# Performance work log

Hardware: AMD Instinct MI355X
Metric: run time of the kernel (lower is better)

Reference implementation:

```python
import jax, jax.numpy as jnp
import numpy as np

S, B, I, H, NH, HD, ML = 512, 32, 768, 256, 8, 32, 512
LN_EPS = 1e-5


def setup_inputs() -> dict:
    key = jax.random.key(0)
    ks = jax.random.split(key, 12)
    r = lambda k, shp, s=0.05: jax.random.normal(k, shp, dtype=jnp.float32) * s
    return {
        'x': r(ks[0], (S, B, I), 1.0),
        'Wi': r(ks[1], (5 * H, I)), 'bi': jnp.zeros((5 * H,), jnp.float32),
        'Wh': r(ks[2], (5 * H, H)), 'bh': jnp.zeros((5 * H,), jnp.float32),
        'Wt': r(ks[3], (H, 3 * H)), 'bt': jnp.zeros((H,), jnp.float32),
        'Wq': r(ks[4], (3, H, H)), 'bq': jnp.zeros((3, H), jnp.float32),
        'Wk': r(ks[5], (3, H, H)), 'bk': jnp.zeros((3, H), jnp.float32),
        'Wv': r(ks[6], (3, H, H)), 'bv': jnp.zeros((3, H), jnp.float32),
        'Wo': r(ks[7], (3, H, H)), 'bo': jnp.zeros((3, H), jnp.float32),
        'relpos': r(ks[8], (3, NH, ML, HD), 1.0),
        'ln_g': jnp.ones((H,), jnp.float32), 'ln_b': jnp.zeros((H,), jnp.float32),
    }


def cumsoftmax(z):
    return jnp.cumsum(jax.nn.softmax(z, axis=-1), axis=-1)


def _forward(x, Wi, bi, Wh, bh, Wt, bt, Wq, bq, Wk, bk, Wv, bv, Wo, bo, relpos, ln_g, ln_b):
    # --- sequential PFN (ON-LSTM style) recurrence over time ---
    def step(carry, xt):
        h, c_in = carry
        gates = xt @ Wi.T + bi + h @ Wh.T + bh            # [B, 5H]
        c, eg_cin, rg_cin, eg_c, rg_c = jnp.split(gates, 5, axis=-1)
        eg_cin = 1.0 - cumsoftmax(eg_cin)
        rg_cin = cumsoftmax(rg_cin)
        eg_c = 1.0 - cumsoftmax(eg_c)
        rg_c = cumsoftmax(rg_c)
        c = jnp.tanh(c)
        ov_c = rg_c * eg_c
        up_c = rg_c - ov_c
        dn_c = eg_c - ov_c
        ov_i = rg_cin * eg_cin
        up_i = rg_cin - ov_i
        dn_i = eg_cin - ov_i
        share = ov_i * c_in + ov_c * c
        c_re = up_i * c_in + up_c * c + share
        c_ner = dn_i * c_in + dn_c * c + share
        h_re = jnp.tanh(c_re)
        h_ner = jnp.tanh(c_ner)
        h_share = jnp.tanh(share)
        c_out = jnp.concatenate([c_re, c_ner, share], axis=-1) @ Wt.T + bt
        h_out = jnp.tanh(c_out)
        return (h_out, c_out), (h_ner, h_re, h_share)

    init = (jnp.zeros((B, H), x.dtype), jnp.zeros((B, H), x.dtype))
    _, (h_ner, h_re, h_share) = jax.lax.scan(step, init, x)   # each [S, B, H]

    # --- relative multi-head attention (no 1/sqrt(d) scaling, as in source) ---
    def attn(hb, i):
        b, s, d = hb.shape
        q = (hb @ Wq[i].T + bq[i]).reshape(b, s, NH, HD)
        k = (hb @ Wk[i].T + bk[i]).reshape(b, s, NH, HD)
        v = (hb @ Wv[i].T + bv[i]).reshape(b, s, NH, HD)
        scores = jnp.einsum('bqnd,bknd->bnqk', q, k) \
               + jnp.einsum('bqnd,nkd->bnqk', q, relpos[i][:, :s])
        w = jax.nn.softmax(scores, axis=-1)
        o = jnp.einsum('bnqk,bknd->bqnd', w, v).reshape(b, s, d)
        return o @ Wo[i].T + bo[i]

    def layer_norm(z):
        m = z.mean(-1, keepdims=True)
        v = z.var(-1, keepdims=True)
        return (z - m) / jnp.sqrt(v + LN_EPS) * ln_g + ln_b

    def apply_attention(h_sbd, i):
        hb = jnp.transpose(h_sbd, (1, 0, 2))      # [B, S, H]
        y = layer_norm(hb + attn(hb, i))          # residual + LN (dropout=0, eval)
        return jnp.transpose(y, (1, 0, 2))        # back to [S, B, H]

    out_ner = apply_attention(h_ner, 0)
    out_re = apply_attention(h_re, 1)
    out_share = apply_attention(h_re, 2)  # faithful to source: h_share attn consumes h_re
    return out_ner, out_re, out_share


def reference(x, Wi, bi, Wh, bh, Wt, bt, Wq, bq, Wk, bk, Wv, bv, Wo, bo, relpos, ln_g, ln_b):
    return _forward(x, Wi, bi, Wh, bh, Wt, bt, Wq, bq, Wk, bk, Wv, bv, Wo, bo, relpos, ln_g, ln_b)
```

## Files before the change

kernel.cpp:

```cpp
#include <hip/hip_runtime.h>
#include <hip/hip_bf16.h>

#define SDIM 512
#define BDIM 32

typedef _Float16 v2h __attribute__((ext_vector_type(2)));
typedef short bf16x8 __attribute__((ext_vector_type(8)));
typedef float f32x4 __attribute__((ext_vector_type(4)));

__device__ __forceinline__ float b2f(ushort u) {
    union { uint32_t i; float f; } v; v.i = ((uint32_t)u) << 16; return v.f;
}
__device__ __forceinline__ ushort f2b(float f) {
    union { float f; uint32_t i; } v; v.f = f;
    uint32_t u = v.i;
    return (ushort)((u + 0x7fffu + ((u >> 16) & 1u)) >> 16);
}
__device__ __forceinline__ ushort f2h(float f) {
    union { _Float16 h; ushort u; } v; v.h = (_Float16)f; return v.u;
}
__device__ __forceinline__ float dot2(uint32_t w, uint32_t h, float acc) {
#if __has_builtin(__builtin_amdgcn_fdot2)
    union { uint32_t u; v2h v; } a, b;
    a.u = w; b.u = h;
    return __builtin_amdgcn_fdot2(a.v, b.v, acc, false);
#else
    union { uint32_t u; v2h v; } a, b;
    a.u = w; b.u = h;
    return acc + (float)a.v.x * (float)b.v.x + (float)a.v.y * (float)b.v.y;
#endif
}
__device__ __forceinline__ float ftanh(float x) {
    const float t = __expf(2.f * x);
    return 1.f - 2.f * __builtin_amdgcn_rcpf(t + 1.f);
}

#define DCHUNK8C(WQ, HQ, ACC)                                                  \
    {                                                                          \
        uint4 wA = *(const uint4*)(WQ);                                        \
        uint4 wB = *(const uint4*)((WQ) + 4);                                  \
        uint4 hA = *(const uint4*)(HQ);                                        \
        uint4 hB = *(const uint4*)((HQ) + 4);                                  \
        ACC = dot2(wA.x, hA.x, ACC);                                           \
        ACC = dot2(wA.y, hA.y, ACC);                                           \
        ACC = dot2(wA.z, hA.z, ACC);                                           \
        ACC = dot2(wA.w, hA.w, ACC);                                           \
        ACC = dot2(wB.x, hB.x, ACC);                                           \
        ACC = dot2(wB.y, hB.y, ACC);                                           \
        ACC = dot2(wB.z, hB.z, ACC);                                           \
        ACC = dot2(wB.w, hB.w, ACC);                                           \
    }

__global__ __launch_bounds__(256) void pack8d_kernel(
    const float* __restrict__ src, int ld, uint32_t* __restrict__ out, int P, int J)
{
    const int idx = blockIdx.x * 256 + threadIdx.x;
    if (idx >= P * J) return;
    const int j = idx / P, p = idx - j * P;
    const ushort lo = f2h(src[(size_t)j * ld + 2 * p]);
    const ushort hi = f2h(src[(size_t)j * ld + 2 * p + 1]);
    out[(((size_t)(p >> 3) * J + j) << 3) + (p & 7)] = ((uint32_t)hi << 16) | lo;
}

__global__ __launch_bounds__(256) void cvt_bf16x2_kernel(
    const float* __restrict__ a, ushort* __restrict__ oa, int na,
    const float* __restrict__ b, ushort* __restrict__ ob, int nb)
{
    const int stride = gridDim.x * 256;
    for (int i = blockIdx.x * 256 + threadIdx.x; i < na + nb; i += stride) {
        if (i < na) oa[i] = f2b(a[i]);
        else ob[i - na] = f2b(b[i - na]);
    }
}
__global__ __launch_bounds__(256) void cvt_bf16x4_kernel(
    const float* __restrict__ a, const float* __restrict__ b,
    const float* __restrict__ c, const float* __restrict__ d,
    ushort* __restrict__ oa, ushort* __restrict__ ob,
    ushort* __restrict__ oc, ushort* __restrict__ od, int n)
{
    const int i = blockIdx.x * 256 + threadIdx.x;
    if (i >= 4 * n) return;
    const int which = i / n, j = i - which * n;
    const float* s = which == 0 ? a : which == 1 ? b : which == 2 ? c : d;
    ushort* o = which == 0 ? oa : which == 1 ? ob : which == 2 ? oc : od;
    o[j] = f2b(s[j]);
}

__global__ __launch_bounds__(256) void addvec_kernel(
    const float* __restrict__ a, const float* __restrict__ b,
    float* __restrict__ o, int n)
{
    const int i = blockIdx.x * 256 + threadIdx.x;
    if (i < n) o[i] = a[i] + b[i];
}

__global__ __launch_bounds__(256) void mfma_gemm128_kernel(
    const ushort* __restrict__ A16, const ushort* __restrict__ B16,
    const float* __restrict__ bias, float* __restrict__ C, int N, int K)
{
    __shared__ ushort As[128][72];
    __shared__ ushort Bs[64][72];
    const int tid = threadIdx.x;
    const int tile_m = blockIdx.x * 128, tile_n = blockIdx.y * 64;
    const int ra = tid >> 1, ca = (tid & 1) * 32;
    const int rb = tid >> 2, cb = (tid & 3) * 16;
    const int w = tid >> 6, lane = tid & 63;
    const int mi = lane & 15, quad = lane >> 4;
    f32x4 acc[2][4] = {};

    for (int k0 = 0; k0 < K; k0 += 64) {
        const uint4* ap = (const uint4*)(A16 + (size_t)(tile_m + ra) * K + k0 + ca);
        *(uint4*)&As[ra][ca]      = ap[0];
        *(uint4*)&As[ra][ca + 8]  = ap[1];
        *(uint4*)&As[ra][ca + 16] = ap[2];
        *(uint4*)&As[ra][ca + 24] = ap[3];
        const uint4* bp = (const uint4*)(B16 + (size_t)(tile_n + rb) * K + k0 + cb);
        *(uint4*)&Bs[rb][cb]     = bp[0];
        *(uint4*)&Bs[rb][cb + 8] = bp[1];
        __syncthreads();
        #pragma unroll
        for (int kk = 0; kk < 64; kk += 32) {
            const bf16x8 af0 = *(const bf16x8*)&As[w * 32 + mi][quad * 8 + kk];
            const bf16x8 af1 = *(const bf16x8*)&As[w * 32 + 16 + mi][quad * 8 + kk];
            #pragma unroll
            for (int j = 0; j < 4; j++) {
                const bf16x8 bf = *(const bf16x8*)&Bs[j * 16 + mi][quad * 8 + kk];
                acc[0][j] = __builtin_amdgcn_mfma_f32_16x16x32_bf16(af0, bf, acc[0][j], 0, 0, 0);
                acc[1][j] = __builtin_amdgcn_mfma_f32_16x16x32_bf16(af1, bf, acc[1][j], 0, 0, 0);
            }
        }
        __syncthreads();
    }
    #pragma unroll
    for (int j = 0; j < 4; j++) {
        const int gn = tile_n + j * 16 + mi;
        const float bv = bias[gn];
        #pragma unroll
        for (int f = 0; f < 2; f++) {
            #pragma unroll
            for (int rr = 0; rr < 4; rr++) {
                const int gm = tile_m + w * 32 + f * 16 + quad * 4 + rr;
                C[(size_t)gm * N + gn] = acc[f][j][rr] + bv;
            }
        }
    }
}

__global__ __launch_bounds__(256) void qkv_gemm128_kernel(
    const ushort* __restrict__ A16,
    const ushort* __restrict__ Wq, const ushort* __restrict__ Wk,
    const ushort* __restrict__ Wv,
    const float* __restrict__ bq, const float* __restrict__ bk,
    const float* __restrict__ bv, const float* __restrict__ rp,
    float* __restrict__ qo, float* __restrict__ ko, float* __restrict__ vo)
{
    __shared__ ushort As[128][72];
    __shared__ ushort Bs[3][64][72];
    const int tid = threadIdx.x;
    const int tile_m = blockIdx.x * 128, tile_n = blockIdx.y * 64;
    const int ra = tid >> 1, ca = (tid & 1) * 32;
    const int am = tile_m + ra;
    const int ar = (am & (SDIM - 1)) * BDIM + (am >> 9);
    const int rb = tid >> 2, cb = (tid & 3) * 16;
    const int bn = tile_n + rb;
    const int w = tid >> 6, lane = tid & 63;
    const int mi = lane & 15, quad = lane >> 4;
    f32x4 acc[3][2][4] = {};

    for (int k0 = 0; k0 < 256; k0 += 64) {
        const uint4* ap = (const uint4*)(A16 + (size_t)ar * 256 + k0 + ca);
        *(uint4*)&As[ra][ca]      = ap[0];
        *(uint4*)&As[ra][ca + 8]  = ap[1];
        *(uint4*)&As[ra][ca + 16] = ap[2];
        *(uint4*)&As[ra][ca + 24] = ap[3];
        const uint4* qp = (const uint4*)(Wq + (size_t)bn * 256 + k0 + cb);
        *(uint4*)&Bs[0][rb][cb]     = qp[0];
        *(uint4*)&Bs[0][rb][cb + 8] = qp[1];
        const uint4* kp = (const uint4*)(Wk + (size_t)bn * 256 + k0 + cb);
        *(uint4*)&Bs[1][rb][cb]     = kp[0];
        *(uint4*)&Bs[1][rb][cb + 8] = kp[1];
        const uint4* vp = (const uint4*)(Wv + (size_t)bn * 256 + k0 + cb);
        *(uint4*)&Bs[2][rb][cb]     = vp[0];
        *(uint4*)&Bs[2][rb][cb + 8] = vp[1];
        __syncthreads();
        #pragma unroll
        for (int kk = 0; kk < 64; kk += 32) {
            const bf16x8 af0 = *(const bf16x8*)&As[w * 32 + mi][quad * 8 + kk];
            const bf16x8 af1 = *(const bf16x8*)&As[w * 32 + 16 + mi][quad * 8 + kk];
            #pragma unroll
            for (int z = 0; z < 3; z++) {
                #pragma unroll
                for (int j = 0; j < 4; j++) {
                    const bf16x8 bf = *(const bf16x8*)&Bs[z][j * 16 + mi][quad * 8 + kk];
                    acc[z][0][j] = __builtin_amdgcn_mfma_f32_16x16x32_bf16(af0, bf, acc[z][0][j], 0, 0, 0);
                    acc[z][1][j] = __builtin_amdgcn_mfma_f32_16x16x32_bf16(af1, bf, acc[z][1][j], 0, 0, 0);
                }
            }
        }
        __syncthreads();
    }
    #pragma unroll
    for (int z = 0; z < 3; z++) {
        const float* bias = (z == 0) ? bq : (z == 1) ? bk : bv;
        float* out = (z == 0) ? qo : (z == 1) ? ko : vo;
        #pragma unroll
        for (int j = 0; j < 4; j++) {
            const int gn = tile_n + j * 16 + mi;
            const float bb = bias[gn];
            #pragma unroll
            for (int f = 0; f < 2; f++) {
                #pragma unroll
                for (int rr = 0; rr < 4; rr++) {
                    const int gm = tile_m + w * 32 + f * 16 + quad * 4 + rr;
                    float v = acc[z][f][j][rr] + bb;
                    if (z == 1) {
                        const int sgm = gm & (SDIM - 1);
                        v += rp[((gn >> 5) << 14) + (sgm << 5) + (gn & 31)];
                    }
                    out[(size_t)gm * 256 + gn] = v;
                }
            }
        }
    }
}

__global__ __launch_bounds__(1024) void scan_kernel(
    const float* __restrict__ gx,
    const uint32_t* __restrict__ Wh8,
    const uint32_t* __restrict__ Wt8,
    const float* __restrict__ bt,
    ushort* __restrict__ h_ner,
    ushort* __restrict__ h_re)
{
    const int b = blockIdx.x;
    const int tid = threadIdx.x;
    __shared__ float cs[256], g[1280], ext[1024];
    __shared__ alignas(16) uint32_t hs_pk[128];
    __shared__ alignas(16) uint32_t cat_pk[384];
    __shared__ float rsum[16];
    if (tid < 256) cs[tid] = 0.f;
    if (tid < 128) hs_pk[tid] = 0u;
    __syncthreads();
    const int lane = tid & 63;
    const int ch = tid >> 8;
    const int wch = (tid >> 6) & 3;
    const int er = tid & 255;
    const int ep = tid >> 8;
    const uint32_t* wmain = Wh8 + (size_t)tid * 8;
    const uint32_t* wext  = Wh8 + ((size_t)(ep * 4) * 1280 + 1024 + er) * 8;
    const uint32_t* wtp   = Wt8 + ((size_t)(ep * 12) * 256 + er) * 8;

    for (int t = 0; t < SDIM; t++) {
        const float* gxr = gx + (size_t)(t * BDIM + b) * 1280;
        {
            float a0 = 0.f, a1 = 0.f;
            #pragma unroll 2
            for (int q8 = 0; q8 < 16; q8 += 2) {
                DCHUNK8C(wmain + (size_t)q8 * (1280 * 8), hs_pk + q8 * 8, a0);
                DCHUNK8C(wmain + (size_t)(q8 + 1) * (1280 * 8), hs_pk + q8 * 8 + 8, a1);
            }
            g[tid] = gxr[tid] + a0 + a1;
        }
        {
            float ae = (ep == 0) ? gxr[1024 + er] : 0.f;
            #pragma unroll
            for (int i = 0; i < 4; i++)
                DCHUNK8C(wext + (size_t)i * (1280 * 8), hs_pk + (ep * 4 + i) * 8, ae);
            ext[ep * 256 + er] = ae;
        }
        __syncthreads();
        if (tid < 256) g[tid] = ftanh(g[tid]);
        float v;
        if (tid >= 768) {
            const int r_ = tid - 768;
            v = ext[r_] + ext[256 + r_] + ext[512 + r_] + ext[768 + r_];
        } else {
            v = g[256 + tid];
        }
        const float e = __expf(v);
        float wsum = e;
        #pragma unroll
        for (int off = 32; off >= 1; off >>= 1) wsum += __shfl_xor(wsum, off, 64);
        if (lane == 0) rsum[ch * 4 + wch] = wsum;
        float cum = e;
        #pragma unroll
        for (int off = 1; off <= 32; off <<= 1) {
            float tsh = __shfl_up(cum, (unsigned)off, 64);
            if (lane >= off) cum += tsh;
        }
        __syncthreads();
        const float tot = rsum[ch * 4] + rsum[ch * 4 + 1] + rsum[ch * 4 + 2] + rsum[ch * 4 + 3];
        float prev = 0.f;
        if (wch > 0) prev += rsum[ch * 4];
        if (wch > 1) prev += rsum[ch * 4 + 1];
        if (wch > 2) prev += rsum[ch * 4 + 2];
        float r = (cum + prev) * __builtin_amdgcn_rcpf(tot);
        if (ch == 0 || ch == 2) r = 1.f - r;
        g[256 + tid] = r;
        __syncthreads();
        if (tid < 256) {
            const float c = g[tid];
            const float egi = g[256 + tid], rgi = g[512 + tid];
            const float egc = g[768 + tid], rgc = g[1024 + tid];
            const float cin = cs[tid];
            const float ovc = rgc * egc, upc = rgc - ovc, dnc = egc - ovc;
            const float ovi = rgi * egi, upi = rgi - ovi, dni = egi - ovi;
            const float share = ovi * cin + ovc * c;
            const float cre = upi * cin + upc * c + share;
            const float cner = dni * cin + dnc * c + share;
            ((_Float16*)cat_pk)[tid]       = (_Float16)cre;
            ((_Float16*)cat_pk)[256 + tid] = (_Float16)cner;
            ((_Float16*)cat_pk)[512 + tid] = (_Float16)share;
            const size_t ob = (size_t)(t * BDIM + b) * 256 + tid;
            h_re[ob] = f2b(ftanh(cre));
            h_ner[ob] = f2b(ftanh(cner));
        }
        __syncthreads();
        {
            float s0 = 0.f, s1 = 0.f;
            #pragma unroll 2
            for (int i = 0; i < 12; i += 2) {
                DCHUNK8C(wtp + (size_t)i * (256 * 8), cat_pk + (ep * 12 + i) * 8, s0);
                DCHUNK8C(wtp + (size_t)(i + 1) * (256 * 8), cat_pk + (ep * 12 + i + 1) * 8, s1);
            }
            g[ep * 256 + er] = s0 + s1;
        }
        __syncthreads();
        if (tid < 256) {
            const float co = g[tid] + g[256 + tid] + g[512 + tid] + g[768 + tid] + bt[tid];
            cs[tid] = co;
            ((_Float16*)hs_pk)[tid] = (_Float16)ftanh(co);
        }
        __syncthreads();
    }
}

__global__ __launch_bounds__(512) void attn_kernel(
    const float* __restrict__ q_ws, const float* __restrict__ kk_ws,
    const float* __restrict__ v_ws, ushort* __restrict__ o16)
{
    __shared__ float sc[8 * 516];
    __shared__ float ps[8 * 256];
    __shared__ float sinv[8];
    const int bn = blockIdx.x;
    const int b = bn >> 3, n = bn & 7;
    const int tid = threadIdx.x;
    const int w = tid >> 6, lane = tid & 63;
    const int ki = w * 64 + lane;
    float kv[32];
    {
        const float4* kp = (const float4*)(kk_ws + (size_t)(b * 512 + ki) * 256 + n * 32);
        #pragma unroll
        for (int d4 = 0; d4 < 8; d4++) {
            float4 x = kp[d4];
            kv[4 * d4] = x.x; kv[4 * d4 + 1] = x.y; kv[4 * d4 + 2] = x.z; kv[4 * d4 + 3] = x.w;
        }
    }
    const int rr = lane >> 3, dq = lane & 7;

    for (int q0 = 0; q0 < 512; q0 += 8) {
        const float* qbase = q_ws + (size_t)(b * 512 + q0) * 256 + n * 32;
        #pragma unroll 1
        for (int r = 0; r < 8; r++) {
            const float4* q4 = (const float4*)(qbase + r * 256);
            float s0 = 0.f, s1 = 0.f;
            #pragma unroll
            for (int d4 = 0; d4 < 8; d4 += 2) {
                const float4 qa = q4[d4];
                const float4 qb = q4[d4 + 1];
                s0 += qa.x * kv[4 * d4] + qa.y * kv[4 * d4 + 1]
                    + qa.z * kv[4 * d4 + 2] + qa.w * kv[4 * d4 + 3];
                s1 += qb.x * kv[4 * d4 + 4] + qb.y * kv[4 * d4 + 5]
                    + qb.z * kv[4 * d4 + 6] + qb.w * kv[4 * d4 + 7];
            }
            sc[r * 516 + ki] = s0 + s1;
        }
        __syncthreads();
        {
            float* row = sc + w * 516;
            float4 a = ((const float4*)row)[lane];
            float4 c4 = ((const float4*)row)[lane + 64];
            float mx = fmaxf(fmaxf(fmaxf(a.x, a.y), fmaxf(a.z, a.w)),
                             fmaxf(fmaxf(c4.x, c4.y), fmaxf(c4.z, c4.w)));
            #pragma unroll
            for (int off = 32; off >= 1; off >>= 1) mx = fmaxf(mx, __shfl_xor(mx, off, 64));
            a.x = __expf(a.x - mx); a.y = __expf(a.y - mx);
            a.z = __expf(a.z - mx); a.w = __expf(a.w - mx);
            c4.x = __expf(c4.x - mx); c4.y = __expf(c4.y - mx);
            c4.z = __expf(c4.z - mx); c4.w = __expf(c4.w - mx);
            float sm = a.x + a.y + a.z + a.w + c4.x + c4.y + c4.z + c4.w;
            #pragma unroll
            for (int off = 32; off >= 1; off >>= 1) sm += __shfl_xor(sm, off, 64);
            ((float4*)row)[lane] = a;
            ((float4*)row)[lane + 64] = c4;
            if (lane == 0) sinv[w] = 1.f / sm;
        }
        __syncthreads();
        {
            float4 acc0 = {0.f, 0.f, 0.f, 0.f};
            float4 acc1 = {0.f, 0.f, 0.f, 0.f};
            const float* erow = sc + rr * 516 + w * 64;
            const float* vbase = v_ws + (size_t)(b * 512 + w * 64) * 256 + n * 32 + dq * 4;
            #pragma unroll 4
            for (int j = 0; j < 64; j += 2) {
                const float e0 = erow[j], e1 = erow[j + 1];
                float4 v0 = *(const float4*)(vbase + (size_t)j * 256);
                float4 v1 = *(const float4*)(vbase + (size_t)(j + 1) * 256);
                acc0.x += e0 * v0.x; acc0.y += e0 * v0.y;
                acc0.z += e0 * v0.z; acc0.w += e0 * v0.w;
                acc1.x += e1 * v1.x; acc1.y += e1 * v1.y;
                acc1.z += e1 * v1.z; acc1.w += e1 * v1.w;
            }
            float4 acc = {acc0.x + acc1.x, acc0.y + acc1.y,
                          acc0.z + acc1.z, acc0.w + acc1.w};
            ((float4*)ps)[tid] = acc;
        }
        __syncthreads();
        if (tid < 256) {
            const int r2 = tid >> 5, d = tid & 31;
            float s = 0.f;
            #pragma unroll
            for (int ww = 0; ww < 8; ww++) s += ps[ww * 256 + r2 * 32 + d];
            o16[(size_t)(b * 512 + q0 + r2) * 256 + n * 32 + d] = f2b(s * sinv[r2]);
        }
        __syncthreads();
    }
}

__global__ __launch_bounds__(256) void ln_kernel(
    const float* __restrict__ proj, const ushort* __restrict__ hsrc,
    const float* __restrict__ lng, const float* __restrict__ lnb,
    float* __restrict__ outp)
{
    const int m = blockIdx.x;
    const int j = threadIdx.x;
    const int b = m >> 9, s = m & 511;
    const size_t oidx = (size_t)(s * 32 + b) * 256 + j;
    const float y = proj[(size_t)m * 256 + j] + b2f(hsrc[oidx]);
    float sum = y, sq = y * y;
    #pragma unroll
    for (int off = 32; off >= 1; off >>= 1) {
        sum += __shfl_xor(sum, off, 64);
        sq += __shfl_xor(sq, off, 64);
    }
    __shared__ float r1[4], r2[4];
    const int wv = j >> 6;
    if ((j & 63) == 0) { r1[wv] = sum; r2[wv] = sq; }
    __syncthreads();
    const float ts = r1[0] + r1[1] + r1[2] + r1[3];
    const float tq = r2[0] + r2[1] + r2[2] + r2[3];
    const float mean = ts * (1.f / 256.f);
    const float var = tq * (1.f / 256.f) - mean * mean;
    const float o = (y - mean) * rsqrtf(var + 1e-5f) * lng[j] + lnb[j];
    outp[oidx] = o;
}

extern "C" void kernel_launch(void* const* d_in, const int* in_sizes, int n_in,
                              void* d_out, int out_size, void* d_ws, size_t ws_size,
                              hipStream_t stream) {
    (void)in_sizes; (void)n_in; (void)out_size; (void)ws_size;
    const float* x   = (const float*)d_in[0];
    const float* Wi  = (const float*)d_in[1];
    const float* bi  = (const float*)d_in[2];
    const float* Wh  = (const float*)d_in[3];
    const float* bh  = (const float*)d_in[4];
    const float* Wt  = (const float*)d_in[5];
    const float* bt  = (const float*)d_in[6];
    const float* Wq  = (const float*)d_in[7];
    const float* bq  = (const float*)d_in[8];
    const float* Wk  = (const float*)d_in[9];
    const float* bk  = (const float*)d_in[10];
    const float* Wv  = (const float*)d_in[11];
    const float* bv  = (const float*)d_in[12];
    const float* Wo  = (const float*)d_in[13];
    const float* bo  = (const float*)d_in[14];
    const float* rp  = (const float*)d_in[15];
    const float* lng = (const float*)d_in[16];
    const float* lnb = (const float*)d_in[17];
    float* outp = (float*)d_out;

    float* ws = (float*)d_ws;
    float* gx    = ws;
    float* q_ws  = ws;
    float* kk_ws = ws + 4194304;
    float* v_ws  = ws + 8388608;
    float* pj_ws = ws + 12582912;
    ushort* o16  = (ushort*)(ws + 16777216);
    ushort* hner16 = (ushort*)(ws + 20971520);
    ushort* hre16  = (ushort*)(ws + 23068672);
    uint32_t* Wh8 = (uint32_t*)(ws + 25165824);
    uint32_t* Wt8 = (uint32_t*)(ws + 25329664);
    ushort* Wq16 = (ushort*)(ws + 25427968);
    ushort* Wk16 = (ushort*)(ws + 25526272);
    ushort* Wv16 = (ushort*)(ws + 25624576);
    ushort* Wo16 = (ushort*)(ws + 25722880);

    ushort* x16  = (ushort*)outp;
    ushort* Wi16 = (ushort*)(outp + 6291456);
    float* bsum  = outp + 7307264;

    pack8d_kernel<<<dim3(640), 256, 0, stream>>>(Wh, 256, Wh8, 128, 1280);
    pack8d_kernel<<<dim3(384), 256, 0, stream>>>(Wt, 768, Wt8, 384, 256);
    addvec_kernel<<<dim3(5), 256, 0, stream>>>(bi, bh, bsum, 1280);
    cvt_bf16x2_kernel<<<dim3(4096), 256, 0, stream>>>(x, x16, 12582912, Wi, Wi16, 983040);
    cvt_bf16x4_kernel<<<dim3(3072), 256, 0, stream>>>(
        Wq, Wk, Wv, Wo, Wq16, Wk16, Wv16, Wo16, 196608);

    mfma_gemm128_kernel<<<dim3(128, 20), 256, 0, stream>>>(
        x16, Wi16, bsum, gx, 1280, 768);

    scan_kernel<<<dim3(32), dim3(1024), 0, stream>>>(gx, Wh8, Wt8, bt, hner16, hre16);

    for (int i = 0; i < 3; i++) {
        const ushort* src16 = (i == 0) ? hner16 : hre16;
        qkv_gemm128_kernel<<<dim3(128, 4), 256, 0, stream>>>(
            src16, Wq16 + (size_t)i * 65536, Wk16 + (size_t)i * 65536,
            Wv16 + (size_t)i * 65536, bq + i * 256, bk + i * 256, bv + i * 256,
            rp + (size_t)i * 131072, q_ws, kk_ws, v_ws);
        attn_kernel<<<dim3(256), dim3(512), 0, stream>>>(q_ws, kk_ws, v_ws, o16);
        mfma_gemm128_kernel<<<dim3(128, 4), 256, 0, stream>>>(
            o16, Wo16 + (size_t)i * 65536, bo + i * 256, pj_ws, 256, 256);
        ln_kernel<<<dim3(16384), dim3(256), 0, stream>>>(
            pj_ws, src16, lng, lnb, outp + (size_t)i * 4194304);
    }
}
```

Measured before the change: 5.926 ms.

## Fuse output projection with residual LayerNorm and split attention queries across blocks

```diff
diff --git a/kernel.cpp b/kernel.cpp
--- a/kernel.cpp
+++ b/kernel.cpp
@@ -220,6 +220,70 @@
                     out[(size_t)gm * 256 + gn] = v;
                 }
             }
+        }
+    }
+}
+
+__global__ __launch_bounds__(256) void oproj_ln_kernel(
+    const ushort* __restrict__ A16,
+    const ushort* __restrict__ W16,
+    const float* __restrict__ bo_, const ushort* __restrict__ hsrc,
+    const float* __restrict__ lng, const float* __restrict__ lnb,
+    float* __restrict__ outp)
+{
+    __shared__ ushort As[64][72];
+    __shared__ ushort Bs[256][72];
+    const int tid = threadIdx.x;
+    const int tile_m = blockIdx.x * 64;
+    const int ra = tid >> 2, ca = (tid & 3) * 16;
+    const int w = tid >> 6, lane = tid & 63;
+    const int mi = lane & 15, quad = lane >> 4;
+    f32x4 acc[16] = {};
+
+    for (int k0 = 0; k0 < 256; k0 += 64) {
+        const uint4* ap = (const uint4*)(A16 + (size_t)(tile_m + ra) * 256 + k0 + ca);
+        *(uint4*)&As[ra][ca]     = ap[0];
+        *(uint4*)&As[ra][ca + 8] = ap[1];
+        const uint4* bp = (const uint4*)(W16 + (size_t)tid * 256 + k0);
+        #pragma unroll
+        for (int u = 0; u < 8; u++)
+            *(uint4*)&Bs[tid][u * 8] = bp[u];
+        __syncthreads();
+        #pragma unroll
+        for (int kk = 0; kk < 64; kk += 32) {
+            const bf16x8 af = *(const bf16x8*)&As[w * 16 + mi][quad * 8 + kk];
+            #pragma unroll
+            for (int j = 0; j < 16; j++) {
+                const bf16x8 bf = *(const bf16x8*)&Bs[j * 16 + mi][quad * 8 + kk];
+                acc[j] = __builtin_amdgcn_mfma_f32_16x16x32_bf16(af, bf, acc[j], 0, 0, 0);
+            }
+        }
+        __syncthreads();
+    }
+    #pragma unroll
+    for (int rr = 0; rr < 4; rr++) {
+        const int gm = tile_m + w * 16 + quad * 4 + rr;
+        const size_t sb = (size_t)((gm & (SDIM - 1)) * BDIM + (gm >> 9)) * 256;
+        float y[16];
+        float sum = 0.f, sq = 0.f;
+        #pragma unroll
+        for (int j = 0; j < 16; j++) {
+            const int col = j * 16 + mi;
+            const float v = acc[j][rr] + bo_[col] + b2f(hsrc[sb + col]);
+            y[j] = v; sum += v; sq += v * v;
+        }
+        #pragma unroll
+        for (int off = 8; off >= 1; off >>= 1) {
+            sum += __shfl_xor(sum, off, 64);
+            sq  += __shfl_xor(sq, off, 64);
+        }
+        const float mean = sum * (1.f / 256.f);
+        const float var = sq * (1.f / 256.f) - mean * mean;
+        const float rs = rsqrtf(var + 1e-5f);
+        #pragma unroll
+        for (int j = 0; j < 16; j++) {
+            const int col = j * 16 + mi;
+            outp[sb + col] = (y[j] - mean) * rs * lng[col] + lnb[col];
         }
     }
 }
@@ -342,8 +406,9 @@
     __shared__ float sc[8 * 516];
     __shared__ float ps[8 * 256];
     __shared__ float sinv[8];
-    const int bn = blockIdx.x;
-    const int b = bn >> 3, n = bn & 7;
+    const int b = blockIdx.x >> 4;
+    const int n = (blockIdx.x >> 1) & 7;
+    const int qh = blockIdx.x & 1;
     const int tid = threadIdx.x;
     const int w = tid >> 6, lane = tid & 63;
     const int ki = w * 64 + lane;
@@ -358,7 +423,7 @@
     }
     const int rr = lane >> 3, dq = lane & 7;
 
-    for (int q0 = 0; q0 < 512; q0 += 8) {
+    for (int q0 = qh * 256; q0 < qh * 256 + 256; q0 += 8) {
         const float* qbase = q_ws + (size_t)(b * 512 + q0) * 256 + n * 32;
         #pragma unroll 1
         for (int r = 0; r < 8; r++) {
@@ -425,34 +490,6 @@
         }
         __syncthreads();
     }
-}
-
-__global__ __launch_bounds__(256) void ln_kernel(
-    const float* __restrict__ proj, const ushort* __restrict__ hsrc,
-    const float* __restrict__ lng, const float* __restrict__ lnb,
-    float* __restrict__ outp)
-{
-    const int m = blockIdx.x;
-    const int j = threadIdx.x;
-    const int b = m >> 9, s = m & 511;
-    const size_t oidx = (size_t)(s * 32 + b) * 256 + j;
-    const float y = proj[(size_t)m * 256 + j] + b2f(hsrc[oidx]);
-    float sum = y, sq = y * y;
-    #pragma unroll
-    for (int off = 32; off >= 1; off >>= 1) {
-        sum += __shfl_xor(sum, off, 64);
-        sq += __shfl_xor(sq, off, 64);
-    }
-    __shared__ float r1[4], r2[4];
-    const int wv = j >> 6;
-    if ((j & 63) == 0) { r1[wv] = sum; r2[wv] = sq; }
-    __syncthreads();
-    const float ts = r1[0] + r1[1] + r1[2] + r1[3];
-    const float tq = r2[0] + r2[1] + r2[2] + r2[3];
-    const float mean = ts * (1.f / 256.f);
-    const float var = tq * (1.f / 256.f) - mean * mean;
-    const float o = (y - mean) * rsqrtf(var + 1e-5f) * lng[j] + lnb[j];
-    outp[oidx] = o;
 }
 
 extern "C" void kernel_launch(void* const* d_in, const int* in_sizes, int n_in,
@@ -484,7 +521,6 @@
     float* q_ws  = ws;
     float* kk_ws = ws + 4194304;
     float* v_ws  = ws + 8388608;
-    float* pj_ws = ws + 12582912;
     ushort* o16  = (ushort*)(ws + 16777216);
     ushort* hner16 = (ushort*)(ws + 20971520);
     ushort* hre16  = (ushort*)(ws + 23068672);
@@ -517,10 +553,9 @@
             src16, Wq16 + (size_t)i * 65536, Wk16 + (size_t)i * 65536,
             Wv16 + (size_t)i * 65536, bq + i * 256, bk + i * 256, bv + i * 256,
             rp + (size_t)i * 131072, q_ws, kk_ws, v_ws);
-        attn_kernel<<<dim3(256), dim3(512), 0, stream>>>(q_ws, kk_ws, v_ws, o16);
-        mfma_gemm128_kernel<<<dim3(128, 4), 256, 0, stream>>>(
-            o16, Wo16 + (size_t)i * 65536, bo + i * 256, pj_ws, 256, 256);
-        ln_kernel<<<dim3(16384), dim3(256), 0, stream>>>(
-            pj_ws, src16, lng, lnb, outp + (size_t)i * 4194304);
-    }
-}
+        attn_kernel<<<dim3(512), dim3(512), 0, stream>>>(q_ws, kk_ws, v_ws, o16);
+        oproj_ln_kernel<<<dim3(256), dim3(256), 0, stream>>>(
+            o16, Wo16 + (size_t)i * 65536, bo + i * 256, src16,
+            lng, lnb, outp + (size_t)i * 4194304);
+    }
+}
```

New measurement: 5.702 ms. -3.8%, faster.
